# Kernel optimization log

Hardware: AMD Instinct MI355X
Metric: run time of the kernel (lower is better)

The kernel has to match this reference:

```python
import jax, jax.numpy as jnp
import numpy as np

V, N, C, DIM, DSPAN, H = 200000, 16384, 16, 300, 512, 150


def setup_inputs() -> dict:
    key = jax.random.key(0)
    ks = jax.random.split(key, 6)
    span_vecs = jax.random.normal(ks[0], (1, N, DSPAN), jnp.float32)
    candidates = jax.random.randint(ks[1], (1, N, C), 0, V)
    # binary candidate mask; guarantee every span has at least one candidate
    mask = (jax.random.uniform(ks[2], (1, N, C)) > 0.3).astype(jnp.float32)
    mask = mask.at[..., 0].set(1.0)
    embed_table = jax.random.normal(ks[3], (V, DIM), jnp.float32) * 0.1
    W1 = jax.random.normal(ks[4], (DSPAN + DIM, H), jnp.float32) * (1.0 / np.sqrt(DSPAN + DIM))
    b1 = jnp.zeros((H,), jnp.float32)
    W2 = jax.random.normal(ks[5], (H, 1), jnp.float32) * (1.0 / np.sqrt(H))
    b2 = jnp.zeros((1,), jnp.float32)
    return dict(span_vecs=span_vecs, candidates=candidates, mask_candidates=mask,
                embed_table=embed_table, W1=W1, b1=b1, W2=W2, b2=b2)


def reference(span_vecs, candidates, mask_candidates, embed_table, W1, b1, W2, b2):
    # gather candidate entity embeddings: [N, C, dim]
    cand_emb = embed_table[candidates[0]]
    sv = span_vecs[0]                                  # [N, Dspan]
    n, c = cand_emb.shape[0], cand_emb.shape[1]
    spans_exp = jnp.broadcast_to(sv[:, None, :], (n, c, sv.shape[-1]))
    ment = jnp.concatenate([spans_exp, cand_emb], axis=-1)  # [N, C, Dspan+dim]
    # 2-layer attention MLP scorer
    h = jax.nn.relu(ment @ W1 + b1)                    # [N, C, H]
    scores = (h @ W2 + b2)[..., 0]                     # [N, C]
    # masked softmax over candidates (log(0) = -inf masks out)
    scores = jax.nn.softmax(scores + jnp.log(mask_candidates[0]), axis=-1)
    # weighted sum of candidate embeddings
    weighted = jnp.einsum('ncd,nc->nd', cand_emb, scores)   # [N, dim]
    # pad span_vecs with dim zeros then scatter weighted into last dim slots
    # == concat since every span has candidates here
    out = jnp.concatenate([sv, weighted], axis=-1)[None]    # [1, N, Dspan+dim]
    return out
```

## Files before the change

### kernel.cpp

```cpp
#include <hip/hip_runtime.h>
#include <hip/hip_bf16.h>
#include <math.h>

#define NSPANS 16384
#define CC     16
#define DIM    300
#define DSPAN  512
#define HH     150
#define HP     160
#define DMENT  812
#define KP     320
#define BSTR   328

typedef short bf16x8 __attribute__((ext_vector_type(8)));
typedef float f32x4  __attribute__((ext_vector_type(4)));

__device__ __forceinline__ unsigned short f2bf(float f) {
    union { float f; unsigned int u; } v; v.f = f;
    unsigned int r = (v.u + 0x7FFFu + ((v.u >> 16) & 1u)) >> 16;
    return (unsigned short)r;
}

__global__ __launch_bounds__(256) void k0_prep(const float* __restrict__ W1,
                                               unsigned short* __restrict__ Wt) {
    int idx = blockIdx.x * 256 + threadIdx.x;
    int n = idx / KP, k = idx - n * KP;
    float v = (n < HH && k < DIM) ? W1[(size_t)(DSPAN + k) * HH + n] : 0.f;
    Wt[idx] = f2bf(v);
}

__global__ __launch_bounds__(512) void k1_span(const float* __restrict__ sv,
                                               const float* __restrict__ W1,
                                               const float* __restrict__ b1,
                                               float* __restrict__ out) {
    const int b  = blockIdx.x;
    const int t  = threadIdx.x;
    const int n0 = b * 32;
    const int team = t >> 8;
    const int u    = t & 255;

    __shared__ float svc_t[2][32][36];
    __shared__ float w1c[2][32][HP];
    __shared__ float partial[32][HP];

    #pragma unroll
    for (int i = 0; i < 8; ++i) {
        int idx4 = t + i * 512;
        int r = idx4 >> 7, c4 = idx4 & 127;
        float4 v = *(const float4*)(sv + (size_t)(n0 + r) * DSPAN + c4 * 4);
        *(float4*)(out + (size_t)(n0 + r) * DMENT + c4 * 4) = v;
    }

    const int tc = u & 31;
    const int tr = u >> 5;
    const int j0 = tc * 5;
    const int r0 = tr * 4;
    const int kbase = team * 256;

    float acc[4][5];
    #pragma unroll
    for (int i = 0; i < 4; ++i)
        #pragma unroll
        for (int j = 0; j < 5; ++j) acc[i][j] = 0.f;

    for (int k0 = 0; k0 < 256; k0 += 32) {
        __syncthreads();
        {
            int r = u >> 3, c4 = u & 7;
            float4 v = *(const float4*)(sv + (size_t)(n0 + r) * DSPAN + kbase + k0 + c4 * 4);
            svc_t[team][c4 * 4 + 0][r] = v.x;
            svc_t[team][c4 * 4 + 1][r] = v.y;
            svc_t[team][c4 * 4 + 2][r] = v.z;
            svc_t[team][c4 * 4 + 3][r] = v.w;
        }
        #pragma unroll
        for (int i = 0; i < 20; ++i) {
            int idx = u + i * 256;
            int k = idx / HP, j = idx - (idx / HP) * HP;
            w1c[team][k][j] = (j < HH) ? W1[(size_t)(kbase + k0 + k) * HH + j] : 0.f;
        }
        __syncthreads();
        #pragma unroll
        for (int kk = 0; kk < 32; ++kk) {
            float4 a4 = *(const float4*)&svc_t[team][kk][r0];
            #pragma unroll
            for (int j = 0; j < 5; ++j) {
                float w = w1c[team][kk][j0 + j];
                acc[0][j] += a4.x * w;
                acc[1][j] += a4.y * w;
                acc[2][j] += a4.z * w;
                acc[3][j] += a4.w * w;
            }
        }
    }

    if (team == 1) {
        #pragma unroll
        for (int i = 0; i < 4; ++i)
            #pragma unroll
            for (int j = 0; j < 5; ++j)
                partial[r0 + i][j0 + j] = acc[i][j];
    }
    __syncthreads();
    if (team == 0) {
        #pragma unroll
        for (int i = 0; i < 4; ++i)
            #pragma unroll
            for (int j = 0; j < 5; ++j) {
                int jj = j0 + j;
                if (jj < HH)
                    out[(size_t)(n0 + r0 + i) * DMENT + DSPAN + jj] =
                        (acc[i][j] + partial[r0 + i][jj]) + b1[jj];
            }
    }
}

__global__ __launch_bounds__(1024) void k2_mfma(const int*   __restrict__ cand,
                                                const float* __restrict__ mask,
                                                const float* __restrict__ emb,
                                                const unsigned short* __restrict__ Wt,
                                                const float* __restrict__ W2,
                                                float*       __restrict__ out) {
    const int b  = blockIdx.x;
    const int t  = threadIdx.x;
    const int n0 = b * 16;
    const int w  = t >> 6;
    const int l  = t & 63;
    const int sp = l & 15;
    const int g  = l >> 4;

    __shared__ unsigned short B_lds[160][BSTR];
    __shared__ float hsL[16][HP];
    __shared__ float w2L[HP];
    __shared__ int   candL[256];
    __shared__ float maskL[256];
    __shared__ float pL[16][16];

    if (t < 256) {
        candL[t] = cand[n0 * CC + t];
        maskL[t] = mask[n0 * CC + t];
    }
    for (int idx = t; idx < 16 * HP; idx += 1024) {
        int s = idx / HP, j = idx - s * HP;
        hsL[s][j] = (j < HH) ? out[(size_t)(n0 + s) * DMENT + DSPAN + j] : 0.f;
    }
    if (t < HP) w2L[t] = (t < HH) ? W2[t] : 0.f;
    for (int idx = t; idx < 6400; idx += 1024) {
        int row = idx / 40, seg = idx - (idx / 40) * 40;
        uint4 v = *(const uint4*)(Wt + (size_t)row * KP + seg * 8);
        *(uint4*)&B_lds[row][seg * 8] = v;
    }
    __syncthreads();

    const float* asrc = emb + (size_t)candL[w * 16 + sp] * DIM;

    float4 abuf[2][2];
    #pragma unroll
    for (int h = 0; h < 2; ++h) {
        abuf[0][h] = *(const float4*)(asrc + g * 8 + h * 4);
        abuf[1][h] = *(const float4*)(asrc + 32 + g * 8 + h * 4);
    }

    f32x4 acc[10];
    #pragma unroll
    for (int nt = 0; nt < 10; ++nt) acc[nt] = 0.f;

    #pragma unroll
    for (int kt = 0; kt < 10; ++kt) {
        const int cur = kt & 1;
        union { uint4 u; bf16x8 h8; } cv;
        cv.u.x = f2bf(abuf[cur][0].x) | ((unsigned)f2bf(abuf[cur][0].y) << 16);
        cv.u.y = f2bf(abuf[cur][0].z) | ((unsigned)f2bf(abuf[cur][0].w) << 16);
        cv.u.z = f2bf(abuf[cur][1].x) | ((unsigned)f2bf(abuf[cur][1].y) << 16);
        cv.u.w = f2bf(abuf[cur][1].z) | ((unsigned)f2bf(abuf[cur][1].w) << 16);
        bf16x8 af = cv.h8;
        if (kt + 2 < 10) {
            #pragma unroll
            for (int h = 0; h < 2; ++h) {
                int kb = (kt + 2) * 32 + g * 8 + h * 4;
                abuf[cur][h] = (kb < DIM) ? *(const float4*)(asrc + kb)
                                          : make_float4(0.f, 0.f, 0.f, 0.f);
            }
        }
        const int koff = kt * 32 + g * 8;
        #pragma unroll
        for (int nt = 0; nt < 10; ++nt) {
            bf16x8 bfr = *(const bf16x8*)&B_lds[nt * 16 + sp][koff];
            acc[nt] = __builtin_amdgcn_mfma_f32_16x16x32_bf16(af, bfr, acc[nt], 0, 0, 0);
        }
    }

    float s0 = 0.f, s1 = 0.f, s2 = 0.f, s3 = 0.f;
    #pragma unroll
    for (int nt = 0; nt < 10; ++nt) {
        int col = nt * 16 + sp;
        float hb  = hsL[w][col];
        float w2v = w2L[col];
        s0 += fmaxf(acc[nt][0] + hb, 0.f) * w2v;
        s1 += fmaxf(acc[nt][1] + hb, 0.f) * w2v;
        s2 += fmaxf(acc[nt][2] + hb, 0.f) * w2v;
        s3 += fmaxf(acc[nt][3] + hb, 0.f) * w2v;
    }
    #pragma unroll
    for (int m = 1; m < 16; m <<= 1) {
        s0 += __shfl_xor(s0, m, 64);
        s1 += __shfl_xor(s1, m, 64);
        s2 += __shfl_xor(s2, m, 64);
        s3 += __shfl_xor(s3, m, 64);
    }

    float v0 = (maskL[w * 16 + g * 4 + 0] > 0.f) ? s0 : -INFINITY;
    float v1 = (maskL[w * 16 + g * 4 + 1] > 0.f) ? s1 : -INFINITY;
    float v2 = (maskL[w * 16 + g * 4 + 2] > 0.f) ? s2 : -INFINITY;
    float v3 = (maskL[w * 16 + g * 4 + 3] > 0.f) ? s3 : -INFINITY;
    float mx = fmaxf(fmaxf(v0, v1), fmaxf(v2, v3));
    mx = fmaxf(mx, __shfl_xor(mx, 16, 64));
    mx = fmaxf(mx, __shfl_xor(mx, 32, 64));
    float e0 = expf(v0 - mx), e1 = expf(v1 - mx), e2 = expf(v2 - mx), e3 = expf(v3 - mx);
    float sm = (e0 + e1) + (e2 + e3);
    sm += __shfl_xor(sm, 16, 64);
    sm += __shfl_xor(sm, 32, 64);
    if (sp == 0) {
        pL[w][g * 4 + 0] = e0 / sm;
        pL[w][g * 4 + 1] = e1 / sm;
        pL[w][g * 4 + 2] = e2 / sm;
        pL[w][g * 4 + 3] = e3 / sm;
    }

    for (int q = l; q < 75; q += 64) {
        float4 a4 = make_float4(0.f, 0.f, 0.f, 0.f);
        #pragma unroll
        for (int c = 0; c < CC; ++c) {
            float p = pL[w][c];
            const float* rp = emb + (size_t)candL[w * 16 + c] * DIM;
            float4 v = *(const float4*)(rp + q * 4);
            a4.x += p * v.x; a4.y += p * v.y; a4.z += p * v.z; a4.w += p * v.w;
        }
        *(float4*)(out + (size_t)(n0 + w) * DMENT + DSPAN + q * 4) = a4;
    }
}

extern "C" void kernel_launch(void* const* d_in, const int* in_sizes, int n_in,
                              void* d_out, int out_size, void* d_ws, size_t ws_size,
                              hipStream_t stream) {
    const float* sv   = (const float*)d_in[0];
    const int*   cand = (const int*)d_in[1];
    const float* mask = (const float*)d_in[2];
    const float* emb  = (const float*)d_in[3];
    const float* W1   = (const float*)d_in[4];
    const float* b1   = (const float*)d_in[5];
    const float* W2   = (const float*)d_in[6];
    float* out = (float*)d_out;
    unsigned short* Wt = (unsigned short*)d_ws;

    k0_prep<<<(HP * KP) / 256, 256, 0, stream>>>(W1, Wt);
    k1_span<<<NSPANS / 32, 512, 0, stream>>>(sv, W1, b1, out);
    k2_mfma<<<NSPANS / 16, 1024, 0, stream>>>(cand, mask, emb, Wt, W2, out);
}
```

Baseline: 586.3 us.

## Rewrite span projection to read pre-transposed W1 directly without LDS tiling

Adds a prep kernel that transposes the span half of W1 into a [160][512] fp32 buffer in workspace. The span GEMV kernel then drops its LDS-staged, split-K two-team scheme and has each thread compute 2 spans by 5 hidden units straight from global memory with float4 loads. Blocks shrink to 16 spans and 256 threads. This removes barriers and LDS traffic but relies on L1/L2 caching for the weight reuse that LDS used to provide.

Result: slower. 739.8 us (+26.2%).

```diff
diff --git a/kernel.cpp b/kernel.cpp
--- a/kernel.cpp
+++ b/kernel.cpp
@@ -29,90 +29,73 @@
     Wt[idx] = f2bf(v);
 }
 
-__global__ __launch_bounds__(512) void k1_span(const float* __restrict__ sv,
-                                               const float* __restrict__ W1,
+__global__ __launch_bounds__(256) void k0b_prep(const float* __restrict__ W1,
+                                                float* __restrict__ W1tT) {
+    int idx = blockIdx.x * 256 + threadIdx.x;
+    int n = idx >> 9, k = idx & 511;
+    W1tT[idx] = (n < HH) ? W1[(size_t)k * HH + n] : 0.f;
+}
+
+__global__ __launch_bounds__(256) void k1_span(const float* __restrict__ sv,
+                                               const float* __restrict__ W1tT,
                                                const float* __restrict__ b1,
                                                float* __restrict__ out) {
     const int b  = blockIdx.x;
     const int t  = threadIdx.x;
-    const int n0 = b * 32;
-    const int team = t >> 8;
-    const int u    = t & 255;
-
-    __shared__ float svc_t[2][32][36];
-    __shared__ float w1c[2][32][HP];
-    __shared__ float partial[32][HP];
+    const int n0 = b * 16;
 
     #pragma unroll
     for (int i = 0; i < 8; ++i) {
-        int idx4 = t + i * 512;
+        int idx4 = t + i * 256;
         int r = idx4 >> 7, c4 = idx4 & 127;
         float4 v = *(const float4*)(sv + (size_t)(n0 + r) * DSPAN + c4 * 4);
         *(float4*)(out + (size_t)(n0 + r) * DMENT + c4 * 4) = v;
     }
 
-    const int tc = u & 31;
-    const int tr = u >> 5;
+    const int tc = t & 31;
+    const int tr = t >> 5;
     const int j0 = tc * 5;
-    const int r0 = tr * 4;
-    const int kbase = team * 256;
-
-    float acc[4][5];
-    #pragma unroll
-    for (int i = 0; i < 4; ++i)
-        #pragma unroll
-        for (int j = 0; j < 5; ++j) acc[i][j] = 0.f;
-
-    for (int k0 = 0; k0 < 256; k0 += 32) {
-        __syncthreads();
-        {
-            int r = u >> 3, c4 = u & 7;
-            float4 v = *(const float4*)(sv + (size_t)(n0 + r) * DSPAN + kbase + k0 + c4 * 4);
-            svc_t[team][c4 * 4 + 0][r] = v.x;
-            svc_t[team][c4 * 4 + 1][r] = v.y;
-            svc_t[team][c4 * 4 + 2][r] = v.z;
-            svc_t[team][c4 * 4 + 3][r] = v.w;
-        }
-        #pragma unroll
-        for (int i = 0; i < 20; ++i) {
-            int idx = u + i * 256;
-            int k = idx / HP, j = idx - (idx / HP) * HP;
-            w1c[team][k][j] = (j < HH) ? W1[(size_t)(kbase + k0 + k) * HH + j] : 0.f;
-        }
-        __syncthreads();
-        #pragma unroll
-        for (int kk = 0; kk < 32; ++kk) {
-            float4 a4 = *(const float4*)&svc_t[team][kk][r0];
-            #pragma unroll
-            for (int j = 0; j < 5; ++j) {
-                float w = w1c[team][kk][j0 + j];
-                acc[0][j] += a4.x * w;
-                acc[1][j] += a4.y * w;
-                acc[2][j] += a4.z * w;
-                acc[3][j] += a4.w * w;
-            }
-        }
-    }
-
-    if (team == 1) {
-        #pragma unroll
-        for (int i = 0; i < 4; ++i)
-            #pragma unroll
-            for (int j = 0; j < 5; ++j)
-                partial[r0 + i][j0 + j] = acc[i][j];
-    }
-    __syncthreads();
-    if (team == 0) {
-        #pragma unroll
-        for (int i = 0; i < 4; ++i)
-            #pragma unroll
-            for (int j = 0; j < 5; ++j) {
-                int jj = j0 + j;
-                if (jj < HH)
-                    out[(size_t)(n0 + r0 + i) * DMENT + DSPAN + jj] =
-                        (acc[i][j] + partial[r0 + i][jj]) + b1[jj];
-            }
-    }
+    const int s0 = tr * 2;
+
+    const float4* a0 = (const float4*)(sv + (size_t)(n0 + s0) * DSPAN);
+    const float4* a1 = (const float4*)(sv + (size_t)(n0 + s0 + 1) * DSPAN);
+    const float4* w0 = (const float4*)(W1tT + (size_t)(j0 + 0) * DSPAN);
+    const float4* w1 = (const float4*)(W1tT + (size_t)(j0 + 1) * DSPAN);
+    const float4* w2 = (const float4*)(W1tT + (size_t)(j0 + 2) * DSPAN);
+    const float4* w3 = (const float4*)(W1tT + (size_t)(j0 + 3) * DSPAN);
+    const float4* w4 = (const float4*)(W1tT + (size_t)(j0 + 4) * DSPAN);
+
+    float acc[2][5];
+    #pragma unroll
+    for (int s = 0; s < 2; ++s)
+        #pragma unroll
+        for (int j = 0; j < 5; ++j) acc[s][j] = 0.f;
+
+    #pragma unroll 2
+    for (int kq = 0; kq < 128; ++kq) {
+        float4 x0 = a0[kq];
+        float4 x1 = a1[kq];
+        float4 wv0 = w0[kq], wv1 = w1[kq], wv2 = w2[kq], wv3 = w3[kq], wv4 = w4[kq];
+        acc[0][0] += x0.x*wv0.x; acc[0][0] += x0.y*wv0.y; acc[0][0] += x0.z*wv0.z; acc[0][0] += x0.w*wv0.w;
+        acc[0][1] += x0.x*wv1.x; acc[0][1] += x0.y*wv1.y; acc[0][1] += x0.z*wv1.z; acc[0][1] += x0.w*wv1.w;
+        acc[0][2] += x0.x*wv2.x; acc[0][2] += x0.y*wv2.y; acc[0][2] += x0.z*wv2.z; acc[0][2] += x0.w*wv2.w;
+        acc[0][3] += x0.x*wv3.x; acc[0][3] += x0.y*wv3.y; acc[0][3] += x0.z*wv3.z; acc[0][3] += x0.w*wv3.w;
+        acc[0][4] += x0.x*wv4.x; acc[0][4] += x0.y*wv4.y; acc[0][4] += x0.z*wv4.z; acc[0][4] += x0.w*wv4.w;
+        acc[1][0] += x1.x*wv0.x; acc[1][0] += x1.y*wv0.y; acc[1][0] += x1.z*wv0.z; acc[1][0] += x1.w*wv0.w;
+        acc[1][1] += x1.x*wv1.x; acc[1][1] += x1.y*wv1.y; acc[1][1] += x1.z*wv1.z; acc[1][1] += x1.w*wv1.w;
+        acc[1][2] += x1.x*wv2.x; acc[1][2] += x1.y*wv2.y; acc[1][2] += x1.z*wv2.z; acc[1][2] += x1.w*wv2.w;
+        acc[1][3] += x1.x*wv3.x; acc[1][3] += x1.y*wv3.y; acc[1][3] += x1.z*wv3.z; acc[1][3] += x1.w*wv3.w;
+        acc[1][4] += x1.x*wv4.x; acc[1][4] += x1.y*wv4.y; acc[1][4] += x1.z*wv4.z; acc[1][4] += x1.w*wv4.w;
+    }
+
+    #pragma unroll
+    for (int s = 0; s < 2; ++s)
+        #pragma unroll
+        for (int j = 0; j < 5; ++j) {
+            int jj = j0 + j;
+            if (jj < HH)
+                out[(size_t)(n0 + s0 + s) * DMENT + DSPAN + jj] = acc[s][j] + b1[jj];
+        }
 }
 
 __global__ __launch_bounds__(1024) void k2_mfma(const int*   __restrict__ cand,
@@ -252,8 +235,10 @@
     const float* W2   = (const float*)d_in[6];
     float* out = (float*)d_out;
     unsigned short* Wt = (unsigned short*)d_ws;
+    float* W1tT = (float*)((char*)d_ws + 102400);
 
     k0_prep<<<(HP * KP) / 256, 256, 0, stream>>>(W1, Wt);
-    k1_span<<<NSPANS / 32, 512, 0, stream>>>(sv, W1, b1, out);
+    k0b_prep<<<(HP * DSPAN) / 256, 256, 0, stream>>>(W1, W1tT);
+    k1_span<<<NSPANS / 16, 256, 0, stream>>>(sv, W1tT, b1, out);
     k2_mfma<<<NSPANS / 16, 1024, 0, stream>>>(cand, mask, emb, Wt, W2, out);
 }
```
